# Kernel optimization log

Measured on AMD Instinct MI355X. Metric: run time of the kernel, lower is better.

## Reference

```python
import jax, jax.numpy as jnp
import numpy as np

B, T, D, H, R = 4, 4096, 1024, 16, 256
DH = D // H  # 64


def setup_inputs() -> dict:
    key = jax.random.key(0)
    ks = jax.random.split(key, 5)
    s = 0.02
    return {
        "x": jax.random.normal(ks[0], (B, T, D), dtype=jnp.float32),
        "Wq": jax.random.normal(ks[1], (D, D), dtype=jnp.float32) * s,
        "bq": jnp.zeros((D,), dtype=jnp.float32),
        "Wd": jax.random.normal(ks[2], (D, R), dtype=jnp.float32) * s,
        "bd": jnp.zeros((R,), dtype=jnp.float32),
        "Wu": jax.random.normal(ks[3], (R, 2 * D), dtype=jnp.float32) * s,
        "bu": jnp.zeros((2 * D,), dtype=jnp.float32),
        "Wo": jax.random.normal(ks[4], (D, D), dtype=jnp.float32) * s,
        "bo": jnp.zeros((D,), dtype=jnp.float32),
    }


def reference(x, Wq, bq, Wd, bd, Wu, bu, Wo, bo):
    b, t = x.shape[0], x.shape[1]
    # q projection -> (B,T,H,DH)
    q = (x @ Wq + bq).reshape(b, t, H, DH)
    # low-rank KV: down then up -> (B,T,H,2*DH)
    kv = ((x @ Wd + bd) @ Wu + bu).reshape(b, t, H, 2 * DH)
    k, v = kv[..., :DH], kv[..., DH:]
    # elu+1 feature map
    q = jax.nn.elu(q) + 1.0
    k = jax.nn.elu(k) + 1.0
    # linear attention: context = k^T v per head -> (B,H,DH,DH)
    context = jnp.einsum("bthd,bthe->bhde", k, v)
    out = jnp.einsum("bthd,bhde->bthe", q, context)  # (B,T,H,DH)
    # normalizer: q . sum_t(k)
    k_sum = k.sum(axis=1)  # (B,H,DH)
    z = 1.0 / (jnp.einsum("bthd,bhd->bth", q, k_sum) + 1e-6)
    out = out * z[..., None]
    return out.reshape(b, t, D) @ Wo + bo
```

## Files before the change

kernel.cpp:

```cpp
#include <hip/hip_runtime.h>
#include <hip/hip_bf16.h>
#include <cstddef>
#include <cstdint>

#define B_  4
#define T_  4096
#define D_  1024
#define H_  16
#define DH_ 64
#define R_  256
#define BT_ (B_ * T_)
#define TWO_D_ (2 * D_)

typedef __attribute__((ext_vector_type(8))) short short8;
typedef __attribute__((ext_vector_type(4))) float f32x4;

__device__ __forceinline__ float elu1(float x) {
    return x > 0.0f ? x + 1.0f : __expf(x);
}

__device__ __forceinline__ float bf2f(short u) {
    union { uint32_t i; float f; } c;
    c.i = ((uint32_t)(uint16_t)u) << 16;
    return c.f;
}

typedef __attribute__((address_space(1))) void void_g;
typedef __attribute__((address_space(3))) void void_l;
__device__ __forceinline__ void gld_lds16(const void* g, void* l) {
    __builtin_amdgcn_global_load_lds(
        (const void_g*)(uintptr_t)g,
        (void_l*)(uint32_t)(uintptr_t)l,
        16, 0, 0);
}

#define BM 128
#define BN 128
#define BK 32
#define NBUF 5

__device__ __forceinline__ void store_out(float* p, float v) { *p = v; }
__device__ __forceinline__ void store_out(__hip_bfloat16* p, float v) { *p = __float2bfloat16(v); }

template<int EPI, bool BROW, typename OT>
__global__ __launch_bounds__(256) void gemm_bf16(
    const __hip_bfloat16* __restrict__ A,
    const __hip_bfloat16* __restrict__ Bt,
    const float* __restrict__ bias,
    OT* __restrict__ C,
    OT* __restrict__ C2,
    int M, int N, int K)
{
    __shared__ alignas(16) __hip_bfloat16 As[NBUF * BM * BK];
    __shared__ alignas(16) __hip_bfloat16 Bs[NBUF * BN * BK];

    const int nbx = N / BN;
    const int id = blockIdx.x;
    const int strip = id / (8 * nbx);
    const int wi = id % (8 * nbx);
    const int bm = (strip * 8 + (wi & 7)) * BM;
    const int bn = (wi >> 3) * BN;

    const int tid  = threadIdx.x;
    const int lane = tid & 63;
    const int wm   = (tid >> 7) * 64;
    const int wn   = ((tid >> 6) & 1) * 64;
    const int r15  = lane & 15;
    const int kg   = lane >> 4;

    f32x4 acc[4][4] = {};

    const int c0 = tid, c1 = tid + 256;
    const __hip_bfloat16* a0 = A  + (size_t)(bm + (c0 >> 2)) * K + (c0 & 3) * 8;
    const __hip_bfloat16* a1 = A  + (size_t)(bm + (c1 >> 2)) * K + (c1 & 3) * 8;
    const __hip_bfloat16* b0 = Bt + (size_t)(bn + (c0 >> 2)) * K + (c0 & 3) * 8;
    const __hip_bfloat16* b1 = Bt + (size_t)(bn + (c1 >> 2)) * K + (c1 & 3) * 8;

    const int nk = K / BK;

    auto stage = [&](int t) {
        const int buf = t % NBUF;
        __hip_bfloat16* Ad = As + buf * (BM * BK);
        __hip_bfloat16* Bd = Bs + buf * (BN * BK);
        const int k0 = t * BK;
        gld_lds16(a0 + k0, Ad + c0 * 8);
        gld_lds16(a1 + k0, Ad + c1 * 8);
        gld_lds16(b0 + k0, Bd + c0 * 8);
        gld_lds16(b1 + k0, Bd + c1 * 8);
    };

    stage(0); stage(1); stage(2);

    for (int t = 0; t < nk; ++t) {
        if (t + 3 < nk) {
            stage(t + 3);
            asm volatile("s_waitcnt vmcnt(12)\ns_barrier" ::: "memory");
        } else if (t + 2 < nk) {
            asm volatile("s_waitcnt vmcnt(8)\ns_barrier" ::: "memory");
        } else if (t + 1 < nk) {
            asm volatile("s_waitcnt vmcnt(4)\ns_barrier" ::: "memory");
        } else {
            asm volatile("s_waitcnt vmcnt(0)\ns_barrier" ::: "memory");
        }

        const __hip_bfloat16* Asb = As + (t % NBUF) * (BM * BK);
        const __hip_bfloat16* Bsb = Bs + (t % NBUF) * (BN * BK);

        short8 af[4], bf[4];
#pragma unroll
        for (int i = 0; i < 4; ++i) {
            af[i] = *(const short8*)(Asb + (wm + i * 16 + r15) * BK + kg * 8);
            bf[i] = *(const short8*)(Bsb + (wn + i * 16 + r15) * BK + kg * 8);
        }
#pragma unroll
        for (int i = 0; i < 4; ++i)
#pragma unroll
            for (int j = 0; j < 4; ++j)
                acc[i][j] = __builtin_amdgcn_mfma_f32_16x16x32_bf16(af[i], bf[j], acc[i][j], 0, 0, 0);
    }

    const int row0 = bm + wm + (lane >> 4) * 4;

    if (EPI == 3) {
        const bool qreg = (bn < 1024);
#pragma unroll
        for (int j = 0; j < 4; ++j) {
            const int col = bn + wn + j * 16 + r15;
            const float bv = bias[col];
#pragma unroll
            for (int i = 0; i < 4; ++i)
#pragma unroll
                for (int r = 0; r < 4; ++r) {
                    const int row = row0 + i * 16 + r;
                    float v = acc[i][j][r] + bv;
                    if (qreg) {
                        store_out(C + (size_t)row * 1024 + col, elu1(v));
                    } else {
                        store_out(C2 + (size_t)row * 256 + (col - 1024), v);
                    }
                }
        }
        return;
    }

    float brow[4][4];
    if (BROW) {
#pragma unroll
        for (int i = 0; i < 4; ++i)
#pragma unroll
            for (int r = 0; r < 4; ++r) brow[i][r] = bias[row0 + i * 16 + r];
    }
#pragma unroll
    for (int j = 0; j < 4; ++j) {
        const int col = bn + wn + j * 16 + r15;
        const float bv = BROW ? 0.0f : bias[col];
        const bool kp_col = ((col & 127) < 64);
#pragma unroll
        for (int i = 0; i < 4; ++i) {
#pragma unroll
            for (int r = 0; r < 4; ++r) {
                const int row = row0 + i * 16 + r;
                float v = acc[i][j][r] + (BROW ? brow[i][r] : bv);
                if (EPI == 1) v = elu1(v);
                else if (EPI == 2) {
                    const bool kp = BROW ? ((row & 127) < 64) : kp_col;
                    if (kp) v = elu1(v);
                }
                store_out(C + (size_t)row * N + col, v);
            }
        }
    }
}

__global__ __launch_bounds__(256) void cast_bf16_kernel(
    const float* __restrict__ s, __hip_bfloat16* __restrict__ d, int n)
{
    const int i = (blockIdx.x * 256 + threadIdx.x) * 8;
    if (i >= n) return;
    float4 v0 = *(const float4*)(s + i);
    float4 v1 = *(const float4*)(s + i + 4);
    __hip_bfloat16 t[8];
    t[0] = __float2bfloat16(v0.x); t[1] = __float2bfloat16(v0.y);
    t[2] = __float2bfloat16(v0.z); t[3] = __float2bfloat16(v0.w);
    t[4] = __float2bfloat16(v1.x); t[5] = __float2bfloat16(v1.y);
    t[6] = __float2bfloat16(v1.z); t[7] = __float2bfloat16(v1.w);
    *(short8*)(d + i) = *(const short8*)t;
}

__global__ __launch_bounds__(256) void transpose_cast(
    const float* __restrict__ W, __hip_bfloat16* __restrict__ Wt, int K, int N)
{
    __shared__ float t[32][33];
    const int n0 = blockIdx.x * 32, k0 = blockIdx.y * 32;
    const int c = threadIdx.x & 31, r = threadIdx.x >> 5;
#pragma unroll
    for (int rr = r; rr < 32; rr += 8)
        t[rr][c] = W[(size_t)(k0 + rr) * N + n0 + c];
    __syncthreads();
#pragma unroll
    for (int rr = r; rr < 32; rr += 8)
        Wt[(size_t)(n0 + rr) * K + k0 + c] = __float2bfloat16(t[c][rr]);
}

__global__ __launch_bounds__(256) void concat_bias(
    const float* __restrict__ bq, const float* __restrict__ bd,
    float* __restrict__ o)
{
    const int i = blockIdx.x * 256 + threadIdx.x;
    o[i] = (i < 1024) ? bq[i] : bd[i - 1024];
}

#define CHT 512

__global__ __launch_bounds__(256) void ctx_mfma(
    const __hip_bfloat16* __restrict__ kvT, float* __restrict__ ctx,
    float* __restrict__ ksum)
{
    __shared__ alignas(16) unsigned char smem[40960];
    float* red0 = (float*)smem;
    float* red1 = (float*)(smem + 20480);

    const int bh = blockIdx.x >> 3;
    const int chunk = blockIdx.x & 7;
    const int b = bh >> 4;
    const int h = bh & 15;
    const int tid = threadIdx.x;
    const int lane = tid & 63;
    const int w = tid >> 6;
    const int r15 = lane & 15;
    const int kg  = lane >> 4;

    f32x4 acc[4][4] = {};
    f32x4 acc4[4] = {};

    const short one = (short)0x3F80;
    const short8 bfv = (r15 == 0)
        ? (short8){one, one, one, one, one, one, one, one}
        : (short8){0, 0, 0, 0, 0, 0, 0, 0};

    const size_t tbase = (size_t)b * T_ + (size_t)chunk * CHT;
    const __hip_bfloat16* src = kvT + (size_t)(h * 128) * BT_ + tbase;

    for (int it = 0; it < CHT / 128; ++it) {
#pragma unroll
        for (int r = 0; r < 8; ++r) {
            const int c = r * 256 + tid;
            const int s = c >> 9, j = (c >> 2) & 127, u = c & 3;
            gld_lds16(src + (size_t)j * BT_ + it * 128 + s * 32 + u * 8,
                      smem + c * 16);
        }
        __syncthreads();

        const __hip_bfloat16* Ls = (const __hip_bfloat16*)smem;
        short8 af[4], bf[4];
#pragma unroll
        for (int i = 0; i < 4; ++i) {
            af[i] = *(const short8*)(Ls + (w * 128 + i * 16 + r15) * 32 + kg * 8);
            bf[i] = *(const short8*)(Ls + (w * 128 + 64 + i * 16 + r15) * 32 + kg * 8);
        }
#pragma unroll
        for (int i = 0; i < 4; ++i) {
#pragma unroll
            for (int j = 0; j < 4; ++j)
                acc[i][j] = __builtin_amdgcn_mfma_f32_16x16x32_bf16(af[i], bf[j], acc[i][j], 0, 0, 0);
            acc4[i] = __builtin_amdgcn_mfma_f32_16x16x32_bf16(af[i], bfv, acc4[i], 0, 0, 0);
        }
        __syncthreads();
    }

    const int q4 = lane >> 4;
    auto wr = [&](float* reg) {
#pragma unroll
        for (int i = 0; i < 4; ++i) {
#pragma unroll
            for (int r = 0; r < 4; ++r) {
                const int row = i * 16 + q4 * 4 + r;
#pragma unroll
                for (int j = 0; j < 4; ++j) reg[row * 80 + j * 16 + r15] = acc[i][j][r];
                reg[row * 80 + 64 + r15] = acc4[i][r];
            }
        }
    };
    auto rd = [&](const float* reg) {
#pragma unroll
        for (int i = 0; i < 4; ++i) {
#pragma unroll
            for (int r = 0; r < 4; ++r) {
                const int row = i * 16 + q4 * 4 + r;
#pragma unroll
                for (int j = 0; j < 4; ++j) acc[i][j][r] += reg[row * 80 + j * 16 + r15];
                acc4[i][r] += reg[row * 80 + 64 + r15];
            }
        }
    };

    if (w == 1) wr(red0);
    if (w == 3) wr(red1);
    __syncthreads();
    if (w == 0) rd(red0);
    if (w == 2) rd(red1);
    __syncthreads();
    if (w == 2) wr(red0);
    __syncthreads();
    if (w == 0) { rd(red0); wr(red0); }
    __syncthreads();

    float* cdst = ctx + (size_t)bh * 4096;
#pragma unroll
    for (int r = 0; r < 16; ++r) {
        const int idx = r * 256 + tid;
        const int d = idx >> 6, e = idx & 63;
        atomicAdd(cdst + idx, red0[d * 80 + e]);
    }
    if (tid < 64) atomicAdd(ksum + bh * 64 + tid, red0[tid * 80 + 64]);
}

__global__ __launch_bounds__(256) void pack_ctx(
    const float* __restrict__ ctx, __hip_bfloat16* __restrict__ ctxT)
{
    __shared__ float L[64 * 65];
    const int bh = blockIdx.x;
    const int tid = threadIdx.x;
#pragma unroll
    for (int r = 0; r < 16; ++r) {
        const int idx = r * 256 + tid;
        L[(idx >> 6) * 65 + (idx & 63)] = ctx[(size_t)bh * 4096 + idx];
    }
    __syncthreads();
#pragma unroll
    for (int r = 0; r < 16; ++r) {
        const int idx = r * 256 + tid;
        ctxT[(size_t)bh * 4096 + idx] =
            __float2bfloat16(L[(idx & 63) * 65 + (idx >> 6)]);
    }
}

__global__ __launch_bounds__(256) void out_mfma(
    const __hip_bfloat16* __restrict__ qb, const __hip_bfloat16* __restrict__ ctxT,
    const float* __restrict__ ksum, __hip_bfloat16* __restrict__ outb)
{
    __shared__ alignas(16) unsigned char As[256 * 128];
    __shared__ alignas(16) unsigned char Bs[64 * 128];
    __shared__ float ksumL[64];
    __shared__ float zbuf[256];

    const int bh = blockIdx.x >> 4;
    const int tile = blockIdx.x & 15;
    const int b = bh >> 4;
    const int h = bh & 15;
    const int tid = threadIdx.x;
    const int lane = tid & 63;
    const int w = tid >> 6;
    const int r15 = lane & 15;
    const int kg  = lane >> 4;

    const size_t trow0 = (size_t)b * T_ + (size_t)tile * 256;

#pragma unroll
    for (int r = 0; r < 8; ++r) {
        const int c = r * 256 + tid;
        const int row = c >> 3, slot = c & 7, u = slot ^ (row & 7);
        gld_lds16(qb + (trow0 + row) * D_ + h * 64 + u * 8, As + c * 16);
    }
#pragma unroll
    for (int r = 0; r < 2; ++r) {
        const int c = r * 256 + tid;
        const int row = c >> 3, slot = c & 7, u = slot ^ (row & 7);
        gld_lds16(ctxT + (size_t)bh * 4096 + row * 64 + u * 8, Bs + c * 16);
    }
    if (tid < 64) ksumL[tid] = ksum[bh * 64 + tid];
    __syncthreads();

    short8 af[4][2], bf[4][2];
#pragma unroll
    for (int i = 0; i < 4; ++i)
#pragma unroll
        for (int s = 0; s < 2; ++s) {
            const int m = w * 64 + i * 16 + r15;
            const int n = i * 16 + r15;
            const int uk = s * 4 + kg;
            af[i][s] = *(const short8*)(As + m * 128 + ((uk ^ (m & 7)) * 16));
            bf[i][s] = *(const short8*)(Bs + n * 128 + ((uk ^ (n & 7)) * 16));
        }

    f32x4 acc[4][4] = {};
#pragma unroll
    for (int s = 0; s < 2; ++s)
#pragma unroll
        for (int i = 0; i < 4; ++i)
#pragma unroll
            for (int j = 0; j < 4; ++j)
                acc[i][j] = __builtin_amdgcn_mfma_f32_16x16x32_bf16(af[i][s], bf[j][s], acc[i][j], 0, 0, 0);

    float dsum[4];
#pragma unroll
    for (int i = 0; i < 4; ++i) {
        float s0 = 0.0f;
#pragma unroll
        for (int s = 0; s < 2; ++s)
#pragma unroll
            for (int j8 = 0; j8 < 8; ++j8)
                s0 += bf2f(af[i][s][j8]) * ksumL[s * 32 + kg * 8 + j8];
        s0 += __shfl_xor(s0, 16);
        s0 += __shfl_xor(s0, 32);
        dsum[i] = s0;
    }
    if (lane < 16) {
#pragma unroll
        for (int i = 0; i < 4; ++i)
            zbuf[w * 64 + i * 16 + lane] = 1.0f / (dsum[i] + 1e-6f);
    }
    __syncthreads();

    const int q4 = lane >> 4;
#pragma unroll
    for (int i = 0; i < 4; ++i) {
#pragma unroll
        for (int r = 0; r < 4; ++r) {
            const int m = w * 64 + i * 16 + q4 * 4 + r;
            const float z = zbuf[m];
#pragma unroll
            for (int j = 0; j < 4; ++j) {
                outb[(trow0 + m) * D_ + h * 64 + j * 16 + r15] =
                    __float2bfloat16(acc[i][j][r] * z);
            }
        }
    }
}

extern "C" void kernel_launch(void* const* d_in, const int* in_sizes, int n_in,
                              void* d_out, int out_size, void* d_ws, size_t ws_size,
                              hipStream_t stream) {
    const float* x  = (const float*)d_in[0];
    const float* Wq = (const float*)d_in[1];
    const float* bq = (const float*)d_in[2];
    const float* Wd = (const float*)d_in[3];
    const float* bd = (const float*)d_in[4];
    const float* Wu = (const float*)d_in[5];
    const float* bu = (const float*)d_in[6];
    const float* Wo = (const float*)d_in[7];
    const float* bo = (const float*)d_in[8];
    float* out = (float*)d_out;

    __hip_bfloat16* xb    = (__hip_bfloat16*)d_ws;
    __hip_bfloat16* WqdT  = xb    + (size_t)BT_ * D_;
    __hip_bfloat16* WuT   = WqdT  + (size_t)1280 * D_;
    __hip_bfloat16* WoT   = WuT   + (size_t)TWO_D_ * R_;
    __hip_bfloat16* xdb   = WoT   + (size_t)D_ * D_;
    __hip_bfloat16* kvT   = xdb   + (size_t)BT_ * R_;
    __hip_bfloat16* qb    = kvT   + (size_t)TWO_D_ * BT_;
    float* bias_qd = (float*)(qb + (size_t)BT_ * D_);
    float* ctx  = bias_qd + 1280;
    float* ksum = ctx + (size_t)B_ * H_ * DH_ * DH_;
    __hip_bfloat16* ctxT = (__hip_bfloat16*)(ksum + B_ * H_ * DH_);
    __hip_bfloat16* outb = xb;

    hipMemsetAsync(ctx, 0,
        (size_t)(B_ * H_ * DH_ * DH_ + B_ * H_ * DH_) * sizeof(float), stream);

    cast_bf16_kernel<<<(BT_ * D_) / (8 * 256), 256, 0, stream>>>(x, xb, BT_ * D_);
    transpose_cast<<<dim3(D_ / 32, D_ / 32), 256, 0, stream>>>(Wq, WqdT, D_, D_);
    transpose_cast<<<dim3(R_ / 32, D_ / 32), 256, 0, stream>>>(Wd, WqdT + (size_t)D_ * D_, D_, R_);
    transpose_cast<<<dim3(TWO_D_ / 32, R_ / 32), 256, 0, stream>>>(Wu, WuT, R_, TWO_D_);
    transpose_cast<<<dim3(D_ / 32, D_ / 32), 256, 0, stream>>>(Wo, WoT, D_, D_);
    concat_bias<<<5, 256, 0, stream>>>(bq, bd, bias_qd);

    gemm_bf16<3, false, __hip_bfloat16><<<(BT_ / BM) * (1280 / BN), 256, 0, stream>>>(
        xb, WqdT, bias_qd, qb, xdb, BT_, 1280, D_);
    gemm_bf16<2, true, __hip_bfloat16><<<(TWO_D_ / BM) * (BT_ / BN), 256, 0, stream>>>(
        WuT, xdb, bu, kvT, nullptr, TWO_D_, BT_, R_);
    ctx_mfma<<<64 * (T_ / CHT), 256, 0, stream>>>(kvT, ctx, ksum);
    pack_ctx<<<64, 256, 0, stream>>>(ctx, ctxT);
    out_mfma<<<64 * 16, 256, 0, stream>>>(qb, ctxT, ksum, outb);
    gemm_bf16<0, false, float><<<(BT_ / BM) * (D_ / BN), 256, 0, stream>>>(
        outb, WoT, bo, out, nullptr, BT_, D_, D_);
}
```

Measured before the change: 335.3 us.

## Add 256x256-tile 512-thread GEMM and split fused QD projection

```diff
diff --git a/kernel.cpp b/kernel.cpp
--- a/kernel.cpp
+++ b/kernel.cpp
@@ -34,13 +34,151 @@
         16, 0, 0);
 }
 
+__device__ __forceinline__ void store_out(float* p, float v) { *p = v; }
+__device__ __forceinline__ void store_out(__hip_bfloat16* p, float v) { *p = __float2bfloat16(v); }
+
+#define PBM 256
+#define PBN 256
+#define PBK 32
+
+template<int EPI, bool BROW, typename OT>
+__global__ __launch_bounds__(512, 2) void gemm_p2(
+    const __hip_bfloat16* __restrict__ A,
+    const __hip_bfloat16* __restrict__ Bt,
+    const float* __restrict__ bias,
+    OT* __restrict__ C,
+    int M, int N, int K)
+{
+    __shared__ alignas(16) __hip_bfloat16 sm[2 * 4 * PBM * PBK];
+    __hip_bfloat16* Asm = sm;
+    __hip_bfloat16* Bsm = sm + 4 * PBM * PBK;
+
+    const int nbx = N / PBN;
+    const int nbm = M / PBM;
+    const int sh = (nbm < 8) ? nbm : 8;
+    const int id = blockIdx.x;
+    const int strip = id / (sh * nbx);
+    const int wi = id % (sh * nbx);
+    const int bm = (strip * sh + (wi % sh)) * PBM;
+    const int bn = (wi / sh) * PBN;
+
+    const int tid  = threadIdx.x;
+    const int lane = tid & 63;
+    const int w    = tid >> 6;
+    const int wm   = w >> 2;
+    const int wn   = w & 3;
+    const int r15  = lane & 15;
+    const int kg   = lane >> 4;
+
+    const int c0 = tid, c1 = tid + 512;
+    const int rA0 = c0 >> 2, rA1 = c1 >> 2;
+    const int gA0 = (c0 & 3) ^ (rA0 & 3), gA1 = (c1 & 3) ^ (rA1 & 3);
+    const __hip_bfloat16* a0 = A  + (size_t)(bm + rA0) * K + gA0 * 8;
+    const __hip_bfloat16* a1 = A  + (size_t)(bm + rA1) * K + gA1 * 8;
+    const __hip_bfloat16* b0 = Bt + (size_t)(bn + rA0) * K + gA0 * 8;
+    const __hip_bfloat16* b1 = Bt + (size_t)(bn + rA1) * K + gA1 * 8;
+
+    auto stageA = [&](int t) {
+        __hip_bfloat16* d = Asm + (t & 3) * (PBM * PBK);
+        gld_lds16(a0 + t * PBK, d + c0 * 8);
+        gld_lds16(a1 + t * PBK, d + c1 * 8);
+    };
+    auto stageB = [&](int t) {
+        __hip_bfloat16* d = Bsm + (t & 3) * (PBM * PBK);
+        gld_lds16(b0 + t * PBK, d + c0 * 8);
+        gld_lds16(b1 + t * PBK, d + c1 * 8);
+    };
+
+    const int nk = K / PBK;
+    f32x4 acc[8][4] = {};
+
+    stageA(0); stageB(0); stageA(1); stageB(1);
+
+    for (int kt = 0; kt < nk; ++kt) {
+        const __hip_bfloat16* As_ = Asm + (kt & 3) * (PBM * PBK);
+        const __hip_bfloat16* Bs_ = Bsm + (kt & 3) * (PBM * PBK);
+
+        if (kt + 2 < nk) {
+            stageA(kt + 2);
+            asm volatile("s_waitcnt vmcnt(6)" ::: "memory");
+        } else if (kt + 2 == nk) {
+            asm volatile("s_waitcnt vmcnt(4)" ::: "memory");
+        } else {
+            asm volatile("s_waitcnt vmcnt(0)" ::: "memory");
+        }
+        __builtin_amdgcn_s_barrier();
+
+        short8 af[8], bf[4];
+#pragma unroll
+        for (int i = 0; i < 4; ++i) {
+            const int r = wm * 128 + i * 16 + r15;
+            af[i] = *(const short8*)(As_ + r * PBK + ((kg ^ (r & 3)) * 8));
+        }
+#pragma unroll
+        for (int j = 0; j < 4; ++j) {
+            const int r = wn * 64 + j * 16 + r15;
+            bf[j] = *(const short8*)(Bs_ + r * PBK + ((kg ^ (r & 3)) * 8));
+        }
+        __builtin_amdgcn_s_setprio(1);
+#pragma unroll
+        for (int i = 0; i < 4; ++i)
+#pragma unroll
+            for (int j = 0; j < 4; ++j)
+                acc[i][j] = __builtin_amdgcn_mfma_f32_16x16x32_bf16(af[i], bf[j], acc[i][j], 0, 0, 0);
+        __builtin_amdgcn_s_setprio(0);
+        __builtin_amdgcn_s_barrier();
+
+        if (kt + 2 < nk) stageB(kt + 2);
+#pragma unroll
+        for (int i = 4; i < 8; ++i) {
+            const int r = wm * 128 + i * 16 + r15;
+            af[i] = *(const short8*)(As_ + r * PBK + ((kg ^ (r & 3)) * 8));
+        }
+        __builtin_amdgcn_s_setprio(1);
+#pragma unroll
+        for (int i = 4; i < 8; ++i)
+#pragma unroll
+            for (int j = 0; j < 4; ++j)
+                acc[i][j] = __builtin_amdgcn_mfma_f32_16x16x32_bf16(af[i], bf[j], acc[i][j], 0, 0, 0);
+        __builtin_amdgcn_s_setprio(0);
+        __builtin_amdgcn_s_barrier();
+    }
+
+    const int row0 = bm + wm * 128 + (lane >> 4) * 4;
+
+    float brow[8][4];
+    if (BROW) {
+#pragma unroll
+        for (int i = 0; i < 8; ++i)
+#pragma unroll
+            for (int r = 0; r < 4; ++r) brow[i][r] = bias[row0 + i * 16 + r];
+    }
+#pragma unroll
+    for (int j = 0; j < 4; ++j) {
+        const int col = bn + wn * 64 + j * 16 + r15;
+        const float bv = BROW ? 0.0f : bias[col];
+        const bool kp_col = ((col & 127) < 64);
+#pragma unroll
+        for (int i = 0; i < 8; ++i) {
+#pragma unroll
+            for (int r = 0; r < 4; ++r) {
+                const int row = row0 + i * 16 + r;
+                float v = acc[i][j][r] + (BROW ? brow[i][r] : bv);
+                if (EPI == 1) v = elu1(v);
+                else if (EPI == 2) {
+                    const bool kp = BROW ? ((row & 127) < 64) : kp_col;
+                    if (kp) v = elu1(v);
+                }
+                store_out(C + (size_t)row * N + col, v);
+            }
+        }
+    }
+}
+
 #define BM 128
 #define BN 128
 #define BK 32
 #define NBUF 5
-
-__device__ __forceinline__ void store_out(float* p, float v) { *p = v; }
-__device__ __forceinline__ void store_out(__hip_bfloat16* p, float v) { *p = __float2bfloat16(v); }
 
 template<int EPI, bool BROW, typename OT>
 __global__ __launch_bounds__(256) void gemm_bf16(
@@ -202,14 +340,6 @@
         Wt[(size_t)(n0 + rr) * K + k0 + c] = __float2bfloat16(t[c][rr]);
 }
 
-__global__ __launch_bounds__(256) void concat_bias(
-    const float* __restrict__ bq, const float* __restrict__ bd,
-    float* __restrict__ o)
-{
-    const int i = blockIdx.x * 256 + threadIdx.x;
-    o[i] = (i < 1024) ? bq[i] : bd[i - 1024];
-}
-
 #define CHT 512
 
 __global__ __launch_bounds__(256) void ctx_mfma(
@@ -463,15 +593,16 @@
     transpose_cast<<<dim3(R_ / 32, D_ / 32), 256, 0, stream>>>(Wd, WqdT + (size_t)D_ * D_, D_, R_);
     transpose_cast<<<dim3(TWO_D_ / 32, R_ / 32), 256, 0, stream>>>(Wu, WuT, R_, TWO_D_);
     transpose_cast<<<dim3(D_ / 32, D_ / 32), 256, 0, stream>>>(Wo, WoT, D_, D_);
-    concat_bias<<<5, 256, 0, stream>>>(bq, bd, bias_qd);
-
-    gemm_bf16<3, false, __hip_bfloat16><<<(BT_ / BM) * (1280 / BN), 256, 0, stream>>>(
-        xb, WqdT, bias_qd, qb, xdb, BT_, 1280, D_);
-    gemm_bf16<2, true, __hip_bfloat16><<<(TWO_D_ / BM) * (BT_ / BN), 256, 0, stream>>>(
-        WuT, xdb, bu, kvT, nullptr, TWO_D_, BT_, R_);
+
+    gemm_bf16<0, false, __hip_bfloat16><<<(BT_ / BM) * (R_ / BN), 256, 0, stream>>>(
+        xb, WqdT + (size_t)D_ * D_, bd, xdb, nullptr, BT_, R_, D_);
+    gemm_p2<1, false, __hip_bfloat16><<<(BT_ / PBM) * (D_ / PBN), 512, 0, stream>>>(
+        xb, WqdT, bq, qb, BT_, D_, D_);
+    gemm_p2<2, true, __hip_bfloat16><<<(TWO_D_ / PBM) * (BT_ / PBN), 512, 0, stream>>>(
+        WuT, xdb, bu, kvT, TWO_D_, BT_, R_);
     ctx_mfma<<<64 * (T_ / CHT), 256, 0, stream>>>(kvT, ctx, ksum);
     pack_ctx<<<64, 256, 0, stream>>>(ctx, ctxT);
     out_mfma<<<64 * 16, 256, 0, stream>>>(qb, ctxT, ksum, outb);
-    gemm_bf16<0, false, float><<<(BT_ / BM) * (D_ / BN), 256, 0, stream>>>(
-        outb, WoT, bo, out, nullptr, BT_, D_, D_);
-}
+    gemm_p2<0, false, float><<<(BT_ / PBM) * (D_ / PBN), 512, 0, stream>>>(
+        outb, WoT, bo, out, BT_, D_, D_);
+}
```

Result: no change. 336.1 us (+0.2%).
